# Kernel optimization log

Measured on AMD Instinct MI355X. Metric: run time of the kernel, lower is better.

The kernel has to match this reference:

```python
import jax, jax.numpy as jnp
import numpy as np

N, E = 5000, 10000          # nodes, edges
F_IN, F_EDGE = 16, 4        # raw node / edge feature dims
H, EH, HID3 = 96, 16, 32    # node hidden, edge hidden, edge-MLP hidden
T, L, C = 5, 10, 3          # Chebyshev order, num DeepGCN layers, num classes
LN_EPS = 1e-5


def setup_inputs() -> dict:
    key = jax.random.key(0)
    ks = jax.random.split(key, 12)
    x = jax.random.normal(ks[0], (N, F_IN), jnp.float32)
    edge_index = jax.random.randint(ks[1], (2, E), 0, N)
    ea = jax.random.uniform(ks[2], (E, F_EDGE), dtype=jnp.float32)
    # first column is an edge-type flag; ~half the edges are 'sequence' edges (type 0)
    etype = jax.random.randint(ks[3], (E,), 0, 2).astype(jnp.float32)
    edge_attr = ea.at[:, 0].set(etype)

    def glorot(k, sh, fan):
        return jax.random.normal(k, sh, jnp.float32) / np.float32(np.sqrt(fan))

    cheb_w = glorot(ks[4], (T, F_IN, H), F_IN)
    cheb_b = jnp.zeros((H,), jnp.float32)
    enc_w = glorot(ks[5], (F_EDGE, EH), F_EDGE)
    enc_b = jnp.zeros((EH,), jnp.float32)
    # per-layer NNConv edge MLP (MapE2NxN): 16 -> 32 -> 96*96
    mlp_w1 = glorot(ks[6], (L, EH, HID3), EH)
    mlp_b1 = jnp.zeros((L, HID3), jnp.float32)
    mlp_w2 = glorot(ks[7], (L, HID3, H * H), HID3) * 0.1  # keep edge-weight magnitudes sane
    mlp_b2 = jnp.zeros((L, H * H), jnp.float32)
    root = glorot(ks[8], (L, H, H), H)
    conv_b = jnp.zeros((L, H), jnp.float32)
    ln_g = jnp.ones((L, H), jnp.float32)
    ln_b = jnp.zeros((L, H), jnp.float32)
    lin_w = glorot(ks[9], (H, C), H)
    lin_b = jnp.zeros((C,), jnp.float32)
    return dict(x=x, edge_index=edge_index, edge_attr=edge_attr,
                cheb_w=cheb_w, cheb_b=cheb_b, enc_w=enc_w, enc_b=enc_b,
                mlp_w1=mlp_w1, mlp_b1=mlp_b1, mlp_w2=mlp_w2, mlp_b2=mlp_b2,
                root=root, conv_b=conv_b, ln_g=ln_g, ln_b=ln_b,
                lin_w=lin_w, lin_b=lin_b)


def _layer_norm(v, g, b):
    mu = jnp.mean(v, axis=-1, keepdims=True)
    var = jnp.mean((v - mu) ** 2, axis=-1, keepdims=True)
    return (v - mu) * jax.lax.rsqrt(var + LN_EPS) * g + b


def _cheb_conv(x, row, col, mask, W, b):
    # symmetric-normalized Laplacian, lambda_max=2 => L_hat = -D^-1/2 A D^-1/2 (diag 0)
    # mask zeroes out non-sequence edges and self loops (PyG removes self loops)
    deg = jax.ops.segment_sum(mask, row, num_segments=N)
    dinv = jnp.where(deg > 0, deg ** -0.5, 0.0)
    w = -dinv[row] * dinv[col] * mask  # [E]
    Lmul = lambda v: jax.ops.segment_sum(w[:, None] * v[row], col, num_segments=N)
    Tx0 = x
    out = Tx0 @ W[0]
    Tx1 = Lmul(x)
    out = out + Tx1 @ W[1]
    for k in range(2, T):
        Tx2 = 2.0 * Lmul(Tx1) - Tx0
        out = out + Tx2 @ W[k]
        Tx0, Tx1 = Tx1, Tx2
    return out + b


def _nnconv(x, row, col, ea, w1, b1, w2, b2, rt, cb):
    # per-edge weight matrix from edge MLP (dropout in eval mode = identity)
    We = ((ea @ w1 + b1) @ w2 + b2).reshape(E, H, H)
    msg = jnp.einsum('eh,eho->eo', x[row], We)          # gather + per-edge GEMM
    agg = jax.ops.segment_sum(msg, col, num_segments=N)  # scatter-add aggregation
    return agg + x @ rt + cb


def reference(x, edge_index, edge_attr, cheb_w, cheb_b, enc_w, enc_b,
              mlp_w1, mlp_b1, mlp_w2, mlp_b2, root, conv_b, ln_g, ln_b,
              lin_w, lin_b):
    row, col = edge_index[0], edge_index[1]
    # sequence edges (edge type 0), excluding self loops, expressed as a weight mask
    seq_mask = ((edge_attr[:, 0] == 0) & (row != col)).astype(x.dtype)
    h = _cheb_conv(x, row, col, seq_mask, cheb_w, cheb_b)          # node encoder
    ea = edge_attr @ enc_w + enc_b                                  # edge encoder
    # layer 0: conv only
    h = _nnconv(h, row, col, ea, mlp_w1[0], mlp_b1[0], mlp_w2[0], mlp_b2[0],
                root[0], conv_b[0])
    # layers 1..L-1: res+ block (norm -> relu -> [dropout=id] -> conv -> +res)
    for i in range(1, L):
        r = h
        v = jax.nn.relu(_layer_norm(h, ln_g[i], ln_b[i]))
        h = _nnconv(v, row, col, ea, mlp_w1[i], mlp_b1[i], mlp_w2[i], mlp_b2[i],
                    root[i], conv_b[i]) + r
    h = jax.nn.relu(_layer_norm(h, ln_g[0], ln_b[0]))  # layers[0].act(layers[0].norm(x))
    return h @ lin_w + lin_b
```

## Files before the change

kernel.cpp:

```cpp
#include <hip/hip_runtime.h>

#define NN 5000
#define EE 10000
#define F_IN 16
#define F_EDGE 4
#define H 96
#define EHD 16
#define HID3 32
#define T_CHEB 5
#define L_LAYERS 10
#define C_OUT 3
#define LN_EPSF 1e-5f
#define KW 576
#define MD 32
#define BM2 16
#define NBT2 313
#define KC_N 36
#define FRAG_PER_LAYER (6 * KC_N * 64)

typedef float float4v __attribute__((ext_vector_type(4)));
typedef _Float16 half4v __attribute__((ext_vector_type(4)));
typedef _Float16 half8v __attribute__((ext_vector_type(8)));

#if __has_builtin(__builtin_amdgcn_mfma_f32_16x16x16f16)
  #define HAVE_MFMA16 1
  #define MFMA16(a, b, c) __builtin_amdgcn_mfma_f32_16x16x16f16((a), (b), (c), 0, 0, 0)
#elif __has_builtin(__builtin_amdgcn_mfma_f32_16x16x16_f16)
  #define HAVE_MFMA16 1
  #define MFMA16(a, b, c) __builtin_amdgcn_mfma_f32_16x16x16_f16((a), (b), (c), 0, 0, 0)
#else
  #define HAVE_MFMA16 0
  #define MFMA32(a, b, c) __builtin_amdgcn_mfma_f32_16x16x32_f16((a), (b), (c), 0, 0, 0)
#endif

__global__ void k_front(const float* __restrict__ enc_w, const float* __restrict__ enc_b,
                        const float* __restrict__ w1, const float* __restrict__ b1,
                        const float* __restrict__ w2, const float* __restrict__ b2,
                        const float* __restrict__ root,
                        const int* __restrict__ row, const int* __restrict__ col,
                        const float* __restrict__ eattr,
                        _Float16* __restrict__ Mf, float* __restrict__ deg,
                        int* __restrict__ cnt, int* __restrict__ ell_r,
                        float* __restrict__ ell_m, float4* __restrict__ ell_ea) {
    const int tid = blockIdx.x * blockDim.x + threadIdx.x;
    const int NTH = gridDim.x * blockDim.x;
    for (int idx = tid; idx < L_LAYERS * H * H; idx += NTH) {
        int i = idx / (H * H);
        int m = idx % (H * H);
        int h = m / H, o = m % H;
        const float* w2i = w2 + (size_t)i * HID3 * H * H;
        const float* w1i = w1 + i * EHD * HID3;
        float hcol[HID3];
        #pragma unroll
        for (int k2 = 0; k2 < HID3; ++k2) hcol[k2] = w2i[(size_t)k2 * H * H + m];
        float tcol[EHD];
        #pragma unroll
        for (int ke = 0; ke < EHD; ++ke) {
            float s = 0.f;
            #pragma unroll
            for (int k2 = 0; k2 < HID3; ++k2) s += w1i[ke * HID3 + k2] * hcol[k2];
            tcol[ke] = s;
        }
        float vals[6];
        #pragma unroll
        for (int f = 0; f < F_EDGE; ++f) {
            float s = 0.f;
            #pragma unroll
            for (int ke = 0; ke < EHD; ++ke) s += enc_w[f * EHD + ke] * tcol[ke];
            vals[f] = s;
        }
        float c = b2[(size_t)i * H * H + m];
        #pragma unroll
        for (int ke = 0; ke < EHD; ++ke) c += enc_b[ke] * tcol[ke];
        #pragma unroll
        for (int k2 = 0; k2 < HID3; ++k2) c += b1[i * HID3 + k2] * hcol[k2];
        vals[4] = c;
        vals[5] = root[(size_t)i * H * H + m];
        int nt = o >> 4, n15 = o & 15;
        #pragma unroll
        for (int f = 0; f < 6; ++f) {
            int k = f * 96 + h;
            int kc = k >> 4, g2 = (k & 15) >> 2, e2 = k & 3;
            int lane = n15 + 16 * g2;
            Mf[((((size_t)i * 6 + nt) * KC_N + kc) * 64 + lane) * 4 + e2] = (_Float16)vals[f];
        }
    }
    for (int e = tid; e < EE; e += NTH) {
        int r = row[e], c = col[e];
        float4 ea = *(const float4*)(eattr + e * F_EDGE);
        float m = (ea.x == 0.f && r != c) ? 1.f : 0.f;
        if (m != 0.f) atomicAdd(&deg[r], 1.f);
        int slot = atomicAdd(&cnt[c], 1);
        int p = c * MD + slot;
        ell_r[p] = r;
        ell_m[p] = m;
        ell_ea[p] = ea;
    }
}

__global__ void k_cheb_step(const int* __restrict__ cnt, const int* __restrict__ ell_r,
                            const float* __restrict__ ell_m, const float* __restrict__ deg,
                            const float* __restrict__ src, const float* __restrict__ prev,
                            float* __restrict__ dst, float scale) {
    int t = blockIdx.x * blockDim.x + threadIdx.x;
    if (t >= NN * 4) return;
    int c = t >> 2, q = t & 3;
    int n = cnt[c];
    const int* rp = ell_r + c * MD;
    const float* mp = ell_m + c * MD;
    float4 acc = make_float4(0.f, 0.f, 0.f, 0.f);
    for (int p = 0; p < n; ++p) {
        float m = mp[p];
        if (m == 0.f) continue;
        int r = rp[p];
        float w = rsqrtf(deg[r]);
        float4 s = *(const float4*)(src + (size_t)r * F_IN + q * 4);
        acc.x = fmaf(w, s.x, acc.x); acc.y = fmaf(w, s.y, acc.y);
        acc.z = fmaf(w, s.z, acc.z); acc.w = fmaf(w, s.w, acc.w);
    }
    float dc = deg[c];
    float f = dc > 0.f ? -scale * rsqrtf(dc) : 0.f;
    float4 o = make_float4(f * acc.x, f * acc.y, f * acc.z, f * acc.w);
    if (prev) {
        float4 pv = *(const float4*)(prev + (size_t)c * F_IN + q * 4);
        o.x -= pv.x; o.y -= pv.y; o.z -= pv.z; o.w -= pv.w;
    }
    *(float4*)(dst + (size_t)c * F_IN + q * 4) = o;
}

__global__ __launch_bounds__(256) void k_cheb4_out(
        const int* __restrict__ cnt, const int* __restrict__ ell_r,
        const float* __restrict__ ell_m, const float* __restrict__ deg,
        const float* __restrict__ x, const float* __restrict__ T1,
        const float* __restrict__ T2, const float* __restrict__ T3,
        float* __restrict__ T4, const float* __restrict__ cheb_w,
        const float* __restrict__ cheb_b, _Float16* __restrict__ vout) {
    __shared__ float wlds[T_CHEB * F_IN][H];
    const int n0 = blockIdx.x * 64;
    const int t = threadIdx.x;
    for (int i = t; i < T_CHEB * F_IN * H / 4; i += 256)
        ((float4*)wlds)[i] = ((const float4*)cheb_w)[i];
    {
        int c = n0 + (t >> 2), q = t & 3;
        if (c < NN) {
            int n = cnt[c];
            const int* rp = ell_r + c * MD;
            const float* mp = ell_m + c * MD;
            float4 acc = make_float4(0.f, 0.f, 0.f, 0.f);
            for (int p = 0; p < n; ++p) {
                float m = mp[p];
                if (m == 0.f) continue;
                int r = rp[p];
                float w = rsqrtf(deg[r]);
                float4 s = *(const float4*)(T3 + (size_t)r * F_IN + q * 4);
                acc.x = fmaf(w, s.x, acc.x); acc.y = fmaf(w, s.y, acc.y);
                acc.z = fmaf(w, s.z, acc.z); acc.w = fmaf(w, s.w, acc.w);
            }
            float dc = deg[c];
            float f = dc > 0.f ? -2.f * rsqrtf(dc) : 0.f;
            float4 pv = *(const float4*)(T2 + (size_t)c * F_IN + q * 4);
            float4 o = make_float4(f * acc.x - pv.x, f * acc.y - pv.y,
                                   f * acc.z - pv.z, f * acc.w - pv.w);
            *(float4*)(T4 + (size_t)c * F_IN + q * 4) = o;
        }
    }
    __syncthreads();
    {
        int n = n0 + (t >> 2), cseg = t & 3;
        if (n >= NN) return;
        float txv[T_CHEB * F_IN];
        #pragma unroll
        for (int q = 0; q < 4; ++q) {
            *(float4*)(txv + q * 4)      = *(const float4*)(x  + (size_t)n * F_IN + q * 4);
            *(float4*)(txv + 16 + q * 4) = *(const float4*)(T1 + (size_t)n * F_IN + q * 4);
            *(float4*)(txv + 32 + q * 4) = *(const float4*)(T2 + (size_t)n * F_IN + q * 4);
            *(float4*)(txv + 48 + q * 4) = *(const float4*)(T3 + (size_t)n * F_IN + q * 4);
            *(float4*)(txv + 64 + q * 4) = *(const float4*)(T4 + (size_t)n * F_IN + q * 4);
        }
        _Float16* vr = vout + (size_t)n * H + cseg * 24;
        #pragma unroll 4
        for (int c = 0; c < 24; ++c) {
            int o = cseg * 24 + c;
            float s = cheb_b[o];
            #pragma unroll
            for (int kf = 0; kf < T_CHEB * F_IN; ++kf)
                s = fmaf(txv[kf], wlds[kf][o], s);
            vr[c] = (_Float16)s;
        }
    }
}

__global__ __launch_bounds__(128) void k_layer(
        const _Float16* __restrict__ vcur, const float* __restrict__ hres,
        const int* __restrict__ cnt, const int* __restrict__ ell_r,
        const float4* __restrict__ ell_ea, const _Float16* __restrict__ MfL,
        const float* __restrict__ cb, const float* __restrict__ lg,
        const float* __restrict__ lb, const float* __restrict__ lin_w,
        const float* __restrict__ lin_b,
        float* __restrict__ hnext, _Float16* __restrict__ vnext,
        float* __restrict__ outp, int isLast) {
    __shared__ _Float16 zs[BM2][584];
    __shared__ float ho[BM2][100];
    const int n0 = blockIdx.x * BM2;
    const int t = threadIdx.x;

    {
        int r = t >> 3, l8 = t & 7;
        int gn = n0 + r, c0 = l8 * 12;
        float acc[5][12] = {};
        _Float16 selfv[12];
        #pragma unroll
        for (int j = 0; j < 12; ++j) selfv[j] = (_Float16)0.f;
        if (gn < NN) {
            const _Float16* sv = vcur + (size_t)gn * H + c0;
            *(half8v*)(selfv) = *(const half8v*)(sv);
            *(half4v*)(selfv + 8) = *(const half4v*)(sv + 8);
            int nc = cnt[gn];
            const int* rp = ell_r + gn * MD;
            const float4* eap = ell_ea + gn * MD;
            for (int p = 0; p < nc; ++p) {
                int r2 = rp[p];
                float4 ea = eap[p];
                const _Float16* vv = vcur + (size_t)r2 * H + c0;
                half8v v8 = *(const half8v*)vv;
                half4v v4 = *(const half4v*)(vv + 8);
                float vf[12];
                #pragma unroll
                for (int j = 0; j < 8; ++j) vf[j] = (float)v8[j];
                #pragma unroll
                for (int j = 0; j < 4; ++j) vf[8 + j] = (float)v4[j];
                const float cf[4] = {ea.x, ea.y, ea.z, ea.w};
                #pragma unroll
                for (int f = 0; f < 4; ++f)
                    #pragma unroll
                    for (int j = 0; j < 12; ++j)
                        acc[f][j] = fmaf(cf[f], vf[j], acc[f][j]);
                #pragma unroll
                for (int j = 0; j < 12; ++j) acc[4][j] += vf[j];
            }
        }
        #pragma unroll
        for (int f = 0; f < 5; ++f)
            #pragma unroll
            for (int j = 0; j < 12; ++j)
                zs[r][f * 96 + c0 + j] = (_Float16)acc[f][j];
        #pragma unroll
        for (int j = 0; j < 12; ++j) zs[r][480 + c0 + j] = selfv[j];
    }
    __syncthreads();

    const int wid = t >> 6, l = t & 63;
    const int n15 = l & 15, g = l >> 4;
    const half4v* Mf4 = (const half4v*)MfL;
    float4v acc3[3] = {};
#if HAVE_MFMA16
    for (int kc0 = 0; kc0 < KC_N; kc0 += 12) {
        half4v af[12];
        #pragma unroll
        for (int kk = 0; kk < 12; ++kk)
            af[kk] = *(const half4v*)&zs[n15][(kc0 + kk) * 16 + 4 * g];
        #pragma unroll
        for (int j = 0; j < 3; ++j) {
            int nt = wid * 3 + j;
            const half4v* Bp = Mf4 + ((size_t)nt * KC_N + kc0) * 64 + l;
            #pragma unroll
            for (int kk = 0; kk < 12; ++kk)
                acc3[j] = MFMA16(af[kk], Bp[kk * 64], acc3[j]);
        }
    }
#else
    for (int kc0 = 0; kc0 < KC_N; kc0 += 12) {
        half8v af[6];
        #pragma unroll
        for (int kk = 0; kk < 6; ++kk) {
            half4v a0 = *(const half4v*)&zs[n15][(kc0 + 2 * kk) * 16 + 4 * g];
            half4v a1 = *(const half4v*)&zs[n15][(kc0 + 2 * kk + 1) * 16 + 4 * g];
            half8v a;
            #pragma unroll
            for (int e = 0; e < 4; ++e) { a[e] = a0[e]; a[4 + e] = a1[e]; }
            af[kk] = a;
        }
        #pragma unroll
        for (int j = 0; j < 3; ++j) {
            int nt = wid * 3 + j;
            const half4v* Bp = Mf4 + ((size_t)nt * KC_N + kc0) * 64 + l;
            #pragma unroll
            for (int kk = 0; kk < 6; ++kk) {
                half4v b0 = Bp[(2 * kk) * 64];
                half4v b1 = Bp[(2 * kk + 1) * 64];
                half8v b;
                #pragma unroll
                for (int e = 0; e < 4; ++e) { b[e] = b0[e]; b[4 + e] = b1[e]; }
                acc3[j] = MFMA32(af[kk], b, acc3[j]);
            }
        }
    }
#endif
    #pragma unroll
    for (int j = 0; j < 3; ++j) {
        int cc = (wid * 3 + j) * 16 + n15;
        #pragma unroll
        for (int e = 0; e < 4; ++e)
            ho[4 * g + e][cc] = acc3[j][e] + cb[cc];
    }
    __syncthreads();

    {
        int r = t >> 3, l8 = t & 7;
        int gn = n0 + r, c0 = l8 * 12;
        if (gn >= NN) return;
        float hv[12];
        #pragma unroll
        for (int j = 0; j < 12; ++j) hv[j] = ho[r][c0 + j];
        if (hres) {
            const float* rp = hres + (size_t)gn * H + c0;
            #pragma unroll
            for (int j = 0; j < 12; j += 4) {
                float4 rv = *(const float4*)(rp + j);
                hv[j] += rv.x; hv[j + 1] += rv.y; hv[j + 2] += rv.z; hv[j + 3] += rv.w;
            }
        }
        if (!isLast) {
            float* hp = hnext + (size_t)gn * H + c0;
            #pragma unroll
            for (int j = 0; j < 12; j += 4)
                *(float4*)(hp + j) = make_float4(hv[j], hv[j + 1], hv[j + 2], hv[j + 3]);
        }
        float s = 0.f;
        #pragma unroll
        for (int j = 0; j < 12; ++j) s += hv[j];
        s += __shfl_xor(s, 1); s += __shfl_xor(s, 2); s += __shfl_xor(s, 4);
        float mu = s * (1.0f / H);
        float vv = 0.f;
        #pragma unroll
        for (int j = 0; j < 12; ++j) { float d = hv[j] - mu; vv += d * d; }
        vv += __shfl_xor(vv, 1); vv += __shfl_xor(vv, 2); vv += __shfl_xor(vv, 4);
        float is = rsqrtf(vv * (1.0f / H) + LN_EPSF);
        const float* gp = lg + c0;
        const float* bp = lb + c0;
        float yv[12];
        #pragma unroll
        for (int j = 0; j < 12; ++j)
            yv[j] = fmaxf(fmaf((hv[j] - mu) * is, gp[j], bp[j]), 0.f);
        if (!isLast) {
            _Float16 yh[12];
            #pragma unroll
            for (int j = 0; j < 12; ++j) yh[j] = (_Float16)yv[j];
            _Float16* vp = vnext + (size_t)gn * H + c0;
            *(half8v*)vp = *(const half8v*)yh;
            *(half4v*)(vp + 8) = *(const half4v*)(yh + 8);
        } else {
            float a0 = 0.f, a1 = 0.f, a2 = 0.f;
            #pragma unroll
            for (int j = 0; j < 12; ++j) {
                int oo = c0 + j;
                a0 = fmaf(yv[j], lin_w[oo * C_OUT + 0], a0);
                a1 = fmaf(yv[j], lin_w[oo * C_OUT + 1], a1);
                a2 = fmaf(yv[j], lin_w[oo * C_OUT + 2], a2);
            }
            a0 += __shfl_xor(a0, 1); a0 += __shfl_xor(a0, 2); a0 += __shfl_xor(a0, 4);
            a1 += __shfl_xor(a1, 1); a1 += __shfl_xor(a1, 2); a1 += __shfl_xor(a1, 4);
            a2 += __shfl_xor(a2, 1); a2 += __shfl_xor(a2, 2); a2 += __shfl_xor(a2, 4);
            if (l8 == 0) {
                outp[gn * C_OUT + 0] = a0 + lin_b[0];
                outp[gn * C_OUT + 1] = a1 + lin_b[1];
                outp[gn * C_OUT + 2] = a2 + lin_b[2];
            }
        }
    }
}

extern "C" void kernel_launch(void* const* d_in, const int* in_sizes, int n_in,
                              void* d_out, int out_size, void* d_ws, size_t ws_size,
                              hipStream_t stream) {
    const float* x      = (const float*)d_in[0];
    const int*   row    = (const int*)d_in[1];
    const int*   col    = (const int*)d_in[1] + EE;
    const float* eattr  = (const float*)d_in[2];
    const float* cheb_w = (const float*)d_in[3];
    const float* cheb_b = (const float*)d_in[4];
    const float* enc_w  = (const float*)d_in[5];
    const float* enc_b  = (const float*)d_in[6];
    const float* w1     = (const float*)d_in[7];
    const float* b1     = (const float*)d_in[8];
    const float* w2     = (const float*)d_in[9];
    const float* b2     = (const float*)d_in[10];
    const float* root   = (const float*)d_in[11];
    const float* conv_b = (const float*)d_in[12];
    const float* ln_g   = (const float*)d_in[13];
    const float* ln_b   = (const float*)d_in[14];
    const float* lin_w  = (const float*)d_in[15];
    const float* lin_b  = (const float*)d_in[16];

    char* base = (char*)d_ws;
    size_t off = 0;
    auto alloc = [&](size_t nbytes) {
        char* p = base + off;
        off += (nbytes + 255) / 256 * 256;
        return p;
    };
    float*    deg    = (float*)alloc(NN * 4);
    int*      cnt    = (int*)  alloc(NN * 4);
    size_t    ctl_bytes = off;
    _Float16* Mfrag  = (_Float16*)alloc((size_t)L_LAYERS * FRAG_PER_LAYER * 4 * 2);
    float*    TX     = (float*)alloc((size_t)(T_CHEB - 1) * NN * F_IN * 4);
    int*      ell_r  = (int*)  alloc((size_t)NN * MD * 4);
    float*    ell_m  = (float*)alloc((size_t)NN * MD * 4);
    float4*   ell_ea = (float4*)alloc((size_t)NN * MD * 16);
    _Float16* v0     = (_Float16*)alloc((size_t)NN * H * 2);
    _Float16* v1     = (_Float16*)alloc((size_t)NN * H * 2);
    float*    hA     = (float*)alloc((size_t)NN * H * 4);
    float*    hB     = (float*)alloc((size_t)NN * H * 4);
    (void)ws_size; (void)n_in; (void)in_sizes; (void)out_size;

    const int B = 256;
    auto G = [](long n, int b) { return (int)((n + b - 1) / b); };

    hipMemsetAsync(deg, 0, ctl_bytes, stream);
    k_front<<<360, B, 0, stream>>>(enc_w, enc_b, w1, b1, w2, b2, root,
                                   row, col, eattr, Mfrag, deg, cnt, ell_r, ell_m, ell_ea);

    float* T1 = (float*)TX;
    float* T2 = T1 + (size_t)NN * F_IN;
    float* T3 = T2 + (size_t)NN * F_IN;
    float* T4 = T3 + (size_t)NN * F_IN;
    k_cheb_step<<<G((long)NN * 4, B), B, 0, stream>>>(cnt, ell_r, ell_m, deg, x,  nullptr, T1, 1.f);
    k_cheb_step<<<G((long)NN * 4, B), B, 0, stream>>>(cnt, ell_r, ell_m, deg, T1, x,       T2, 2.f);
    k_cheb_step<<<G((long)NN * 4, B), B, 0, stream>>>(cnt, ell_r, ell_m, deg, T2, T1,      T3, 2.f);
    k_cheb4_out<<<G(NN, 64), B, 0, stream>>>(cnt, ell_r, ell_m, deg, x, T1, T2, T3, T4,
                                             cheb_w, cheb_b, v0);

    _Float16* vbuf[2] = { v0, v1 };
    float*    hbuf[2] = { hA, hB };
    for (int li = 0; li < L_LAYERS; ++li) {
        int isLast = (li == L_LAYERS - 1);
        const _Float16* vcur = vbuf[li & 1];
        _Float16*       vnx  = vbuf[(li + 1) & 1];
        const float*    hres = (li > 0) ? hbuf[(li + 1) & 1] : nullptr;
        float*          hnx  = hbuf[li & 1];
        const float* elg = isLast ? ln_g : ln_g + (li + 1) * H;
        const float* elb = isLast ? ln_b : ln_b + (li + 1) * H;
        k_layer<<<NBT2, 128, 0, stream>>>(
            vcur, hres, cnt, ell_r, ell_ea,
            Mfrag + (size_t)li * FRAG_PER_LAYER * 4,
            conv_b + li * H, elg, elb, lin_w, lin_b,
            hnx, vnx, (float*)d_out, isLast);
    }
}
```

Measured before the change: 168.9 us.

## Fuse Chebyshev steps via two-hop gathers and split layer GEMM K across waves

Replaces the four Chebyshev propagation kernels with two kernels. Each computes two recursion levels at once by gathering neighbours-of-neighbours, and T3/T4 stay in shared memory. This removes two launches and the global round trips for T3/T4, at the cost of redundant two-hop gather work. The per-layer kernel now runs 512 threads per block. Eight waves split the 576-deep K dimension into four segments and reduce the partial sums through shared memory. Gather and epilogue work is spread across 256 threads with 6 columns each, giving more parallelism per block at the cost of extra LDS traffic and a reduction step.

```diff
diff --git a/kernel.cpp b/kernel.cpp
--- a/kernel.cpp
+++ b/kernel.cpp
@@ -19,19 +19,11 @@
 #define FRAG_PER_LAYER (6 * KC_N * 64)
 
 typedef float float4v __attribute__((ext_vector_type(4)));
+typedef _Float16 half2v __attribute__((ext_vector_type(2)));
 typedef _Float16 half4v __attribute__((ext_vector_type(4)));
 typedef _Float16 half8v __attribute__((ext_vector_type(8)));
 
-#if __has_builtin(__builtin_amdgcn_mfma_f32_16x16x16f16)
-  #define HAVE_MFMA16 1
-  #define MFMA16(a, b, c) __builtin_amdgcn_mfma_f32_16x16x16f16((a), (b), (c), 0, 0, 0)
-#elif __has_builtin(__builtin_amdgcn_mfma_f32_16x16x16_f16)
-  #define HAVE_MFMA16 1
-  #define MFMA16(a, b, c) __builtin_amdgcn_mfma_f32_16x16x16_f16((a), (b), (c), 0, 0, 0)
-#else
-  #define HAVE_MFMA16 0
-  #define MFMA32(a, b, c) __builtin_amdgcn_mfma_f32_16x16x32_f16((a), (b), (c), 0, 0, 0)
-#endif
+#define MFMA16(a, b, c) __builtin_amdgcn_mfma_f32_16x16x16f16((a), (b), (c), 0, 0, 0)
 
 __global__ void k_front(const float* __restrict__ enc_w, const float* __restrict__ enc_b,
                         const float* __restrict__ w1, const float* __restrict__ b1,
@@ -79,8 +71,8 @@
         int nt = o >> 4, n15 = o & 15;
         #pragma unroll
         for (int f = 0; f < 6; ++f) {
-            int k = f * 96 + h;
-            int kc = k >> 4, g2 = (k & 15) >> 2, e2 = k & 3;
+            int K = f * 96 + h;
+            int kc = K >> 4, g2 = (K & 15) >> 2, e2 = K & 3;
             int lane = n15 + 16 * g2;
             Mf[((((size_t)i * 6 + nt) * KC_N + kc) * 64 + lane) * 4 + e2] = (_Float16)vals[f];
         }
@@ -98,44 +90,61 @@
     }
 }
 
-__global__ void k_cheb_step(const int* __restrict__ cnt, const int* __restrict__ ell_r,
-                            const float* __restrict__ ell_m, const float* __restrict__ deg,
-                            const float* __restrict__ src, const float* __restrict__ prev,
-                            float* __restrict__ dst, float scale) {
+__global__ void k_chebA(const int* __restrict__ cnt, const int* __restrict__ ell_r,
+                        const float* __restrict__ ell_m, const float* __restrict__ deg,
+                        const float* __restrict__ x,
+                        float* __restrict__ T1, float* __restrict__ T2) {
     int t = blockIdx.x * blockDim.x + threadIdx.x;
     if (t >= NN * 4) return;
     int c = t >> 2, q = t & 3;
-    int n = cnt[c];
+    float dc = deg[c];
+    float dinvC = dc > 0.f ? rsqrtf(dc) : 0.f;
+    int nc = cnt[c];
     const int* rp = ell_r + c * MD;
     const float* mp = ell_m + c * MD;
-    float4 acc = make_float4(0.f, 0.f, 0.f, 0.f);
-    for (int p = 0; p < n; ++p) {
-        float m = mp[p];
-        if (m == 0.f) continue;
+    float4 acc1 = make_float4(0.f, 0.f, 0.f, 0.f);
+    float4 acc2 = make_float4(0.f, 0.f, 0.f, 0.f);
+    for (int p = 0; p < nc; ++p) {
+        if (mp[p] == 0.f) continue;
         int r = rp[p];
-        float w = rsqrtf(deg[r]);
-        float4 s = *(const float4*)(src + (size_t)r * F_IN + q * 4);
-        acc.x = fmaf(w, s.x, acc.x); acc.y = fmaf(w, s.y, acc.y);
-        acc.z = fmaf(w, s.z, acc.z); acc.w = fmaf(w, s.w, acc.w);
-    }
-    float dc = deg[c];
-    float f = dc > 0.f ? -scale * rsqrtf(dc) : 0.f;
-    float4 o = make_float4(f * acc.x, f * acc.y, f * acc.z, f * acc.w);
-    if (prev) {
-        float4 pv = *(const float4*)(prev + (size_t)c * F_IN + q * 4);
-        o.x -= pv.x; o.y -= pv.y; o.z -= pv.z; o.w -= pv.w;
-    }
-    *(float4*)(dst + (size_t)c * F_IN + q * 4) = o;
+        float dinvR = rsqrtf(deg[r]);
+        float4 xr = *(const float4*)(x + (size_t)r * F_IN + q * 4);
+        acc1.x = fmaf(dinvR, xr.x, acc1.x); acc1.y = fmaf(dinvR, xr.y, acc1.y);
+        acc1.z = fmaf(dinvR, xr.z, acc1.z); acc1.w = fmaf(dinvR, xr.w, acc1.w);
+        float4 a = make_float4(0.f, 0.f, 0.f, 0.f);
+        int nr = cnt[r];
+        const int* rp2 = ell_r + r * MD;
+        const float* mp2 = ell_m + r * MD;
+        for (int p2 = 0; p2 < nr; ++p2) {
+            if (mp2[p2] == 0.f) continue;
+            int r2 = rp2[p2];
+            float w2v = rsqrtf(deg[r2]);
+            float4 x2 = *(const float4*)(x + (size_t)r2 * F_IN + q * 4);
+            a.x = fmaf(w2v, x2.x, a.x); a.y = fmaf(w2v, x2.y, a.y);
+            a.z = fmaf(w2v, x2.z, a.z); a.w = fmaf(w2v, x2.w, a.w);
+        }
+        float f1 = -dinvR;
+        acc2.x = fmaf(dinvR, f1 * a.x, acc2.x); acc2.y = fmaf(dinvR, f1 * a.y, acc2.y);
+        acc2.z = fmaf(dinvR, f1 * a.z, acc2.z); acc2.w = fmaf(dinvR, f1 * a.w, acc2.w);
+    }
+    float4 xc = *(const float4*)(x + (size_t)c * F_IN + q * 4);
+    float f = -dinvC;
+    *(float4*)(T1 + (size_t)c * F_IN + q * 4) =
+        make_float4(f * acc1.x, f * acc1.y, f * acc1.z, f * acc1.w);
+    float f2 = -2.f * dinvC;
+    *(float4*)(T2 + (size_t)c * F_IN + q * 4) =
+        make_float4(f2 * acc2.x - xc.x, f2 * acc2.y - xc.y,
+                    f2 * acc2.z - xc.z, f2 * acc2.w - xc.w);
 }
 
-__global__ __launch_bounds__(256) void k_cheb4_out(
+__global__ __launch_bounds__(256) void k_chebB(
         const int* __restrict__ cnt, const int* __restrict__ ell_r,
         const float* __restrict__ ell_m, const float* __restrict__ deg,
         const float* __restrict__ x, const float* __restrict__ T1,
-        const float* __restrict__ T2, const float* __restrict__ T3,
-        float* __restrict__ T4, const float* __restrict__ cheb_w,
+        const float* __restrict__ T2, const float* __restrict__ cheb_w,
         const float* __restrict__ cheb_b, _Float16* __restrict__ vout) {
     __shared__ float wlds[T_CHEB * F_IN][H];
+    __shared__ float t34[2][64][F_IN];
     const int n0 = blockIdx.x * 64;
     const int t = threadIdx.x;
     for (int i = t; i < T_CHEB * F_IN * H / 4; i += 256)
@@ -143,30 +152,54 @@
     {
         int c = n0 + (t >> 2), q = t & 3;
         if (c < NN) {
-            int n = cnt[c];
+            float dc = deg[c];
+            float dinvC = dc > 0.f ? rsqrtf(dc) : 0.f;
+            int nc = cnt[c];
             const int* rp = ell_r + c * MD;
             const float* mp = ell_m + c * MD;
-            float4 acc = make_float4(0.f, 0.f, 0.f, 0.f);
-            for (int p = 0; p < n; ++p) {
-                float m = mp[p];
-                if (m == 0.f) continue;
+            float4 a3 = make_float4(0.f, 0.f, 0.f, 0.f);
+            float4 a4 = make_float4(0.f, 0.f, 0.f, 0.f);
+            for (int p = 0; p < nc; ++p) {
+                if (mp[p] == 0.f) continue;
                 int r = rp[p];
-                float w = rsqrtf(deg[r]);
-                float4 s = *(const float4*)(T3 + (size_t)r * F_IN + q * 4);
-                acc.x = fmaf(w, s.x, acc.x); acc.y = fmaf(w, s.y, acc.y);
-                acc.z = fmaf(w, s.z, acc.z); acc.w = fmaf(w, s.w, acc.w);
-            }
-            float dc = deg[c];
-            float f = dc > 0.f ? -2.f * rsqrtf(dc) : 0.f;
-            float4 pv = *(const float4*)(T2 + (size_t)c * F_IN + q * 4);
-            float4 o = make_float4(f * acc.x - pv.x, f * acc.y - pv.y,
-                                   f * acc.z - pv.z, f * acc.w - pv.w);
-            *(float4*)(T4 + (size_t)c * F_IN + q * 4) = o;
+                float dinvR = rsqrtf(deg[r]);
+                float4 t2r = *(const float4*)(T2 + (size_t)r * F_IN + q * 4);
+                a3.x = fmaf(dinvR, t2r.x, a3.x); a3.y = fmaf(dinvR, t2r.y, a3.y);
+                a3.z = fmaf(dinvR, t2r.z, a3.z); a3.w = fmaf(dinvR, t2r.w, a3.w);
+                float4 b = make_float4(0.f, 0.f, 0.f, 0.f);
+                int nr = cnt[r];
+                const int* rp2 = ell_r + r * MD;
+                const float* mp2 = ell_m + r * MD;
+                for (int p2 = 0; p2 < nr; ++p2) {
+                    if (mp2[p2] == 0.f) continue;
+                    int r2 = rp2[p2];
+                    float w2v = rsqrtf(deg[r2]);
+                    float4 t2b = *(const float4*)(T2 + (size_t)r2 * F_IN + q * 4);
+                    b.x = fmaf(w2v, t2b.x, b.x); b.y = fmaf(w2v, t2b.y, b.y);
+                    b.z = fmaf(w2v, t2b.z, b.z); b.w = fmaf(w2v, t2b.w, b.w);
+                }
+                float fr = -2.f * dinvR;
+                float4 t1r = *(const float4*)(T1 + (size_t)r * F_IN + q * 4);
+                float4 t3r = make_float4(fr * b.x - t1r.x, fr * b.y - t1r.y,
+                                         fr * b.z - t1r.z, fr * b.w - t1r.w);
+                a4.x = fmaf(dinvR, t3r.x, a4.x); a4.y = fmaf(dinvR, t3r.y, a4.y);
+                a4.z = fmaf(dinvR, t3r.z, a4.z); a4.w = fmaf(dinvR, t3r.w, a4.w);
+            }
+            float f3 = -2.f * dinvC;
+            float4 t1c = *(const float4*)(T1 + (size_t)c * F_IN + q * 4);
+            float4 t2c = *(const float4*)(T2 + (size_t)c * F_IN + q * 4);
+            int lr = t >> 2;
+            *(float4*)&t34[0][lr][q * 4] =
+                make_float4(f3 * a3.x - t1c.x, f3 * a3.y - t1c.y,
+                            f3 * a3.z - t1c.z, f3 * a3.w - t1c.w);
+            *(float4*)&t34[1][lr][q * 4] =
+                make_float4(f3 * a4.x - t2c.x, f3 * a4.y - t2c.y,
+                            f3 * a4.z - t2c.z, f3 * a4.w - t2c.w);
         }
     }
     __syncthreads();
     {
-        int n = n0 + (t >> 2), cseg = t & 3;
+        int lr = t >> 2, n = n0 + lr, cseg = t & 3;
         if (n >= NN) return;
         float txv[T_CHEB * F_IN];
         #pragma unroll
@@ -174,8 +207,8 @@
             *(float4*)(txv + q * 4)      = *(const float4*)(x  + (size_t)n * F_IN + q * 4);
             *(float4*)(txv + 16 + q * 4) = *(const float4*)(T1 + (size_t)n * F_IN + q * 4);
             *(float4*)(txv + 32 + q * 4) = *(const float4*)(T2 + (size_t)n * F_IN + q * 4);
-            *(float4*)(txv + 48 + q * 4) = *(const float4*)(T3 + (size_t)n * F_IN + q * 4);
-            *(float4*)(txv + 64 + q * 4) = *(const float4*)(T4 + (size_t)n * F_IN + q * 4);
+            *(float4*)(txv + 48 + q * 4) = *(const float4*)&t34[0][lr][q * 4];
+            *(float4*)(txv + 64 + q * 4) = *(const float4*)&t34[1][lr][q * 4];
         }
         _Float16* vr = vout + (size_t)n * H + cseg * 24;
         #pragma unroll 4
@@ -190,7 +223,7 @@
     }
 }
 
-__global__ __launch_bounds__(128) void k_layer(
+__global__ __launch_bounds__(512) void k_layer(
         const _Float16* __restrict__ vcur, const float* __restrict__ hres,
         const int* __restrict__ cnt, const int* __restrict__ ell_r,
         const float4* __restrict__ ell_ea, const _Float16* __restrict__ MfL,
@@ -199,22 +232,21 @@
         const float* __restrict__ lin_b,
         float* __restrict__ hnext, _Float16* __restrict__ vnext,
         float* __restrict__ outp, int isLast) {
-    __shared__ _Float16 zs[BM2][584];
-    __shared__ float ho[BM2][100];
+    __shared__ __align__(16) _Float16 zs[BM2][584];
+    __shared__ float hop[4][BM2][100];
     const int n0 = blockIdx.x * BM2;
     const int t = threadIdx.x;
 
-    {
-        int r = t >> 3, l8 = t & 7;
-        int gn = n0 + r, c0 = l8 * 12;
-        float acc[5][12] = {};
-        _Float16 selfv[12];
-        #pragma unroll
-        for (int j = 0; j < 12; ++j) selfv[j] = (_Float16)0.f;
+    if (t < 256) {
+        int r = t >> 4, lane16 = t & 15;
+        int gn = n0 + r, c0 = lane16 * 6;
+        float accf[5][6] = {};
+        half2v self0 = (half2v)(_Float16)0.f, self1 = self0, self2 = self0;
         if (gn < NN) {
             const _Float16* sv = vcur + (size_t)gn * H + c0;
-            *(half8v*)(selfv) = *(const half8v*)(sv);
-            *(half4v*)(selfv + 8) = *(const half4v*)(sv + 8);
+            self0 = *(const half2v*)(sv + 0);
+            self1 = *(const half2v*)(sv + 2);
+            self2 = *(const half2v*)(sv + 4);
             int nc = cnt[gn];
             const int* rp = ell_r + gn * MD;
             const float4* eap = ell_ea + gn * MD;
@@ -222,146 +254,128 @@
                 int r2 = rp[p];
                 float4 ea = eap[p];
                 const _Float16* vv = vcur + (size_t)r2 * H + c0;
-                half8v v8 = *(const half8v*)vv;
-                half4v v4 = *(const half4v*)(vv + 8);
-                float vf[12];
-                #pragma unroll
-                for (int j = 0; j < 8; ++j) vf[j] = (float)v8[j];
-                #pragma unroll
-                for (int j = 0; j < 4; ++j) vf[8 + j] = (float)v4[j];
+                half2v v0 = *(const half2v*)(vv + 0);
+                half2v v1 = *(const half2v*)(vv + 2);
+                half2v v2 = *(const half2v*)(vv + 4);
+                float vf[6] = {(float)v0[0], (float)v0[1], (float)v1[0],
+                               (float)v1[1], (float)v2[0], (float)v2[1]};
                 const float cf[4] = {ea.x, ea.y, ea.z, ea.w};
                 #pragma unroll
                 for (int f = 0; f < 4; ++f)
                     #pragma unroll
-                    for (int j = 0; j < 12; ++j)
-                        acc[f][j] = fmaf(cf[f], vf[j], acc[f][j]);
+                    for (int j = 0; j < 6; ++j)
+                        accf[f][j] = fmaf(cf[f], vf[j], accf[f][j]);
                 #pragma unroll
-                for (int j = 0; j < 12; ++j) acc[4][j] += vf[j];
-            }
-        }
-        #pragma unroll
-        for (int f = 0; f < 5; ++f)
-            #pragma unroll
-            for (int j = 0; j < 12; ++j)
-                zs[r][f * 96 + c0 + j] = (_Float16)acc[f][j];
-        #pragma unroll
-        for (int j = 0; j < 12; ++j) zs[r][480 + c0 + j] = selfv[j];
+                for (int j = 0; j < 6; ++j) accf[4][j] += vf[j];
+            }
+        }
+        #pragma unroll
+        for (int f = 0; f < 5; ++f) {
+            _Float16* zp = &zs[r][f * 96 + c0];
+            *(half2v*)(zp + 0) = half2v{(_Float16)accf[f][0], (_Float16)accf[f][1]};
+            *(half2v*)(zp + 2) = half2v{(_Float16)accf[f][2], (_Float16)accf[f][3]};
+            *(half2v*)(zp + 4) = half2v{(_Float16)accf[f][4], (_Float16)accf[f][5]};
+        }
+        _Float16* zp = &zs[r][480 + c0];
+        *(half2v*)(zp + 0) = self0;
+        *(half2v*)(zp + 2) = self1;
+        *(half2v*)(zp + 4) = self2;
     }
     __syncthreads();
 
-    const int wid = t >> 6, l = t & 63;
-    const int n15 = l & 15, g = l >> 4;
-    const half4v* Mf4 = (const half4v*)MfL;
-    float4v acc3[3] = {};
-#if HAVE_MFMA16
-    for (int kc0 = 0; kc0 < KC_N; kc0 += 12) {
-        half4v af[12];
-        #pragma unroll
-        for (int kk = 0; kk < 12; ++kk)
-            af[kk] = *(const half4v*)&zs[n15][(kc0 + kk) * 16 + 4 * g];
+    {
+        const int wid = t >> 6, l = t & 63;
+        const int n15 = l & 15, g = l >> 4;
+        const int ntBase = (wid & 1) * 3;
+        const int kSeg = wid >> 1;
+        const int kcBase = kSeg * 9;
+        const half4v* Mf4 = (const half4v*)MfL;
+        half4v af[9];
+        #pragma unroll
+        for (int kk = 0; kk < 9; ++kk)
+            af[kk] = *(const half4v*)&zs[n15][(kcBase + kk) * 16 + 4 * g];
+        float4v acc3[3] = {};
         #pragma unroll
         for (int j = 0; j < 3; ++j) {
-            int nt = wid * 3 + j;
-            const half4v* Bp = Mf4 + ((size_t)nt * KC_N + kc0) * 64 + l;
-            #pragma unroll
-            for (int kk = 0; kk < 12; ++kk)
+            int nt = ntBase + j;
+            const half4v* Bp = Mf4 + ((size_t)nt * KC_N + kcBase) * 64 + l;
+            #pragma unroll
+            for (int kk = 0; kk < 9; ++kk)
                 acc3[j] = MFMA16(af[kk], Bp[kk * 64], acc3[j]);
         }
-    }
-#else
-    for (int kc0 = 0; kc0 < KC_N; kc0 += 12) {
-        half8v af[6];
-        #pragma unroll
-        for (int kk = 0; kk < 6; ++kk) {
-            half4v a0 = *(const half4v*)&zs[n15][(kc0 + 2 * kk) * 16 + 4 * g];
-            half4v a1 = *(const half4v*)&zs[n15][(kc0 + 2 * kk + 1) * 16 + 4 * g];
-            half8v a;
-            #pragma unroll
-            for (int e = 0; e < 4; ++e) { a[e] = a0[e]; a[4 + e] = a1[e]; }
-            af[kk] = a;
-        }
         #pragma unroll
         for (int j = 0; j < 3; ++j) {
-            int nt = wid * 3 + j;
-            const half4v* Bp = Mf4 + ((size_t)nt * KC_N + kc0) * 64 + l;
-            #pragma unroll
-            for (int kk = 0; kk < 6; ++kk) {
-                half4v b0 = Bp[(2 * kk) * 64];
-                half4v b1 = Bp[(2 * kk + 1) * 64];
-                half8v b;
-                #pragma unroll
-                for (int e = 0; e < 4; ++e) { b[e] = b0[e]; b[4 + e] = b1[e]; }
-                acc3[j] = MFMA32(af[kk], b, acc3[j]);
-            }
-        }
-    }
-#endif
-    #pragma unroll
-    for (int j = 0; j < 3; ++j) {
-        int cc = (wid * 3 + j) * 16 + n15;
-        #pragma unroll
-        for (int e = 0; e < 4; ++e)
-            ho[4 * g + e][cc] = acc3[j][e] + cb[cc];
+            int cc = (ntBase + j) * 16 + n15;
+            #pragma unroll
+            for (int e = 0; e < 4; ++e)
+                hop[kSeg][4 * g + e][cc] = acc3[j][e];
+        }
     }
     __syncthreads();
 
-    {
-        int r = t >> 3, l8 = t & 7;
-        int gn = n0 + r, c0 = l8 * 12;
-        if (gn >= NN) return;
-        float hv[12];
-        #pragma unroll
-        for (int j = 0; j < 12; ++j) hv[j] = ho[r][c0 + j];
-        if (hres) {
+    if (t < 256) {
+        int r = t >> 4, lane16 = t & 15;
+        int gn = n0 + r, c0 = lane16 * 6;
+        float hv[6];
+        #pragma unroll
+        for (int j = 0; j < 6; ++j)
+            hv[j] = hop[0][r][c0 + j] + hop[1][r][c0 + j]
+                  + hop[2][r][c0 + j] + hop[3][r][c0 + j] + cb[c0 + j];
+        if (hres && gn < NN) {
             const float* rp = hres + (size_t)gn * H + c0;
             #pragma unroll
-            for (int j = 0; j < 12; j += 4) {
-                float4 rv = *(const float4*)(rp + j);
-                hv[j] += rv.x; hv[j + 1] += rv.y; hv[j + 2] += rv.z; hv[j + 3] += rv.w;
-            }
-        }
-        if (!isLast) {
+            for (int j = 0; j < 6; j += 2) {
+                float2 rv = *(const float2*)(rp + j);
+                hv[j] += rv.x; hv[j + 1] += rv.y;
+            }
+        }
+        if (!isLast && gn < NN) {
             float* hp = hnext + (size_t)gn * H + c0;
             #pragma unroll
-            for (int j = 0; j < 12; j += 4)
-                *(float4*)(hp + j) = make_float4(hv[j], hv[j + 1], hv[j + 2], hv[j + 3]);
+            for (int j = 0; j < 6; j += 2)
+                *(float2*)(hp + j) = make_float2(hv[j], hv[j + 1]);
         }
         float s = 0.f;
         #pragma unroll
-        for (int j = 0; j < 12; ++j) s += hv[j];
-        s += __shfl_xor(s, 1); s += __shfl_xor(s, 2); s += __shfl_xor(s, 4);
+        for (int j = 0; j < 6; ++j) s += hv[j];
+        s += __shfl_xor(s, 1); s += __shfl_xor(s, 2);
+        s += __shfl_xor(s, 4); s += __shfl_xor(s, 8);
         float mu = s * (1.0f / H);
-        float vv = 0.f;
-        #pragma unroll
-        for (int j = 0; j < 12; ++j) { float d = hv[j] - mu; vv += d * d; }
-        vv += __shfl_xor(vv, 1); vv += __shfl_xor(vv, 2); vv += __shfl_xor(vv, 4);
-        float is = rsqrtf(vv * (1.0f / H) + LN_EPSF);
+        float vvr = 0.f;
+        #pragma unroll
+        for (int j = 0; j < 6; ++j) { float d = hv[j] - mu; vvr += d * d; }
+        vvr += __shfl_xor(vvr, 1); vvr += __shfl_xor(vvr, 2);
+        vvr += __shfl_xor(vvr, 4); vvr += __shfl_xor(vvr, 8);
+        float is = rsqrtf(vvr * (1.0f / H) + LN_EPSF);
         const float* gp = lg + c0;
         const float* bp = lb + c0;
-        float yv[12];
-        #pragma unroll
-        for (int j = 0; j < 12; ++j)
+        float yv[6];
+        #pragma unroll
+        for (int j = 0; j < 6; ++j)
             yv[j] = fmaxf(fmaf((hv[j] - mu) * is, gp[j], bp[j]), 0.f);
         if (!isLast) {
-            _Float16 yh[12];
-            #pragma unroll
-            for (int j = 0; j < 12; ++j) yh[j] = (_Float16)yv[j];
-            _Float16* vp = vnext + (size_t)gn * H + c0;
-            *(half8v*)vp = *(const half8v*)yh;
-            *(half4v*)(vp + 8) = *(const half4v*)(yh + 8);
+            if (gn < NN) {
+                _Float16* vp = vnext + (size_t)gn * H + c0;
+                *(half2v*)(vp + 0) = half2v{(_Float16)yv[0], (_Float16)yv[1]};
+                *(half2v*)(vp + 2) = half2v{(_Float16)yv[2], (_Float16)yv[3]};
+                *(half2v*)(vp + 4) = half2v{(_Float16)yv[4], (_Float16)yv[5]};
+            }
         } else {
             float a0 = 0.f, a1 = 0.f, a2 = 0.f;
             #pragma unroll
-            for (int j = 0; j < 12; ++j) {
+            for (int j = 0; j < 6; ++j) {
                 int oo = c0 + j;
                 a0 = fmaf(yv[j], lin_w[oo * C_OUT + 0], a0);
                 a1 = fmaf(yv[j], lin_w[oo * C_OUT + 1], a1);
                 a2 = fmaf(yv[j], lin_w[oo * C_OUT + 2], a2);
             }
-            a0 += __shfl_xor(a0, 1); a0 += __shfl_xor(a0, 2); a0 += __shfl_xor(a0, 4);
-            a1 += __shfl_xor(a1, 1); a1 += __shfl_xor(a1, 2); a1 += __shfl_xor(a1, 4);
-            a2 += __shfl_xor(a2, 1); a2 += __shfl_xor(a2, 2); a2 += __shfl_xor(a2, 4);
-            if (l8 == 0) {
+            a0 += __shfl_xor(a0, 1); a0 += __shfl_xor(a0, 2);
+            a0 += __shfl_xor(a0, 4); a0 += __shfl_xor(a0, 8);
+            a1 += __shfl_xor(a1, 1); a1 += __shfl_xor(a1, 2);
+            a1 += __shfl_xor(a1, 4); a1 += __shfl_xor(a1, 8);
+            a2 += __shfl_xor(a2, 1); a2 += __shfl_xor(a2, 2);
+            a2 += __shfl_xor(a2, 4); a2 += __shfl_xor(a2, 8);
+            if (lane16 == 0 && gn < NN) {
                 outp[gn * C_OUT + 0] = a0 + lin_b[0];
                 outp[gn * C_OUT + 1] = a1 + lin_b[1];
                 outp[gn * C_OUT + 2] = a2 + lin_b[2];
@@ -403,7 +417,8 @@
     int*      cnt    = (int*)  alloc(NN * 4);
     size_t    ctl_bytes = off;
     _Float16* Mfrag  = (_Float16*)alloc((size_t)L_LAYERS * FRAG_PER_LAYER * 4 * 2);
-    float*    TX     = (float*)alloc((size_t)(T_CHEB - 1) * NN * F_IN * 4);
+    float*    T1     = (float*)alloc((size_t)NN * F_IN * 4);
+    float*    T2     = (float*)alloc((size_t)NN * F_IN * 4);
     int*      ell_r  = (int*)  alloc((size_t)NN * MD * 4);
     float*    ell_m  = (float*)alloc((size_t)NN * MD * 4);
     float4*   ell_ea = (float4*)alloc((size_t)NN * MD * 16);
@@ -416,19 +431,12 @@
     const int B = 256;
     auto G = [](long n, int b) { return (int)((n + b - 1) / b); };
 
-    hipMemsetAsync(deg, 0, ctl_bytes, stream);
+    (void)hipMemsetAsync(deg, 0, ctl_bytes, stream);
     k_front<<<360, B, 0, stream>>>(enc_w, enc_b, w1, b1, w2, b2, root,
                                    row, col, eattr, Mfrag, deg, cnt, ell_r, ell_m, ell_ea);
-
-    float* T1 = (float*)TX;
-    float* T2 = T1 + (size_t)NN * F_IN;
-    float* T3 = T2 + (size_t)NN * F_IN;
-    float* T4 = T3 + (size_t)NN * F_IN;
-    k_cheb_step<<<G((long)NN * 4, B), B, 0, stream>>>(cnt, ell_r, ell_m, deg, x,  nullptr, T1, 1.f);
-    k_cheb_step<<<G((long)NN * 4, B), B, 0, stream>>>(cnt, ell_r, ell_m, deg, T1, x,       T2, 2.f);
-    k_cheb_step<<<G((long)NN * 4, B), B, 0, stream>>>(cnt, ell_r, ell_m, deg, T2, T1,      T3, 2.f);
-    k_cheb4_out<<<G(NN, 64), B, 0, stream>>>(cnt, ell_r, ell_m, deg, x, T1, T2, T3, T4,
-                                             cheb_w, cheb_b, v0);
+    k_chebA<<<G((long)NN * 4, B), B, 0, stream>>>(cnt, ell_r, ell_m, deg, x, T1, T2);
+    k_chebB<<<G(NN, 64), B, 0, stream>>>(cnt, ell_r, ell_m, deg, x, T1, T2,
+                                         cheb_w, cheb_b, v0);
 
     _Float16* vbuf[2] = { v0, v1 };
     float*    hbuf[2] = { hA, hB };
@@ -440,7 +448,7 @@
         float*          hnx  = hbuf[li & 1];
         const float* elg = isLast ? ln_g : ln_g + (li + 1) * H;
         const float* elb = isLast ? ln_b : ln_b + (li + 1) * H;
-        k_layer<<<NBT2, 128, 0, stream>>>(
+        k_layer<<<NBT2, 512, 0, stream>>>(
             vcur, hres, cnt, ell_r, ell_ea,
             Mfrag + (size_t)li * FRAG_PER_LAYER * 4,
             conv_b + li * H, elg, elb, lin_w, lin_b,
```

New measurement: 164.6 us. -2.6%, faster.
